# Kernel optimization log

Measured on AMD Instinct MI355X. Metric: run time of the kernel, lower is better.

## Reference

```python
import jax, jax.numpy as jnp
import numpy as np

DIM = 1024
NUM_HEADS = 16
HEAD_DIM = DIM // NUM_HEADS
SEQ = 2048
BATCH = 2


def setup_inputs() -> dict:
    key = jax.random.key(0)
    kx, kq, kk, kv, ko, kb = jax.random.split(key, 6)
    s = 0.02
    return {
        "x": jax.random.normal(kx, (BATCH, SEQ, DIM), dtype=jnp.float32),
        "W_q": jax.random.normal(kq, (DIM, DIM), dtype=jnp.float32) * s,
        "W_k": jax.random.normal(kk, (DIM, DIM), dtype=jnp.float32) * s,
        "W_v": jax.random.normal(kv, (DIM, DIM), dtype=jnp.float32) * s,
        "W_o": jax.random.normal(ko, (DIM, DIM), dtype=jnp.float32) * s,
        "b_o": jax.random.normal(kb, (DIM,), dtype=jnp.float32) * s,
    }


def reference(x, W_q, W_k, W_v, W_o, b_o):
    b, n, d = x.shape
    # Linear layers (torch Linear: y = x @ W.T); weights here stored as [out, in]
    q = jnp.einsum('bnd,ed->bne', x, W_q).reshape(b, n, NUM_HEADS, HEAD_DIM)
    k = jnp.einsum('bnd,ed->bne', x, W_k).reshape(b, n, NUM_HEADS, HEAD_DIM)
    v = jnp.einsum('bnd,ed->bne', x, W_v).reshape(b, n, NUM_HEADS, HEAD_DIM)
    # scores: [b, h, q, k]
    scores = jnp.einsum('bqhd,bkhd->bhqk', q, k)
    causal = jnp.tril(jnp.ones((n, n), dtype=bool))  # True = keep
    scores = jnp.where(causal, scores, -jnp.inf)
    weights = jax.nn.softmax(scores / jnp.sqrt(jnp.float32(HEAD_DIM)), axis=-1)
    ctx = jnp.einsum('bhqk,bkhd->bqhd', weights, v).reshape(b, n, d)
    return jnp.einsum('bnd,ed->bne', ctx, W_o) + b_o
```

## Files before the change

### kernel.cpp

```cpp
#include <hip/hip_runtime.h>
#include <hip/hip_bf16.h>

#define DIM 1024
#define NHEADS 16
#define HD 64
#define SEQ 2048
#define BATCH 2
#define MROWS (BATCH * SEQ)
#define MB (1024u * 1024u)
#define NT (SEQ / 64)

typedef __bf16 bf16x8 __attribute__((ext_vector_type(8)));
typedef float f32x4 __attribute__((ext_vector_type(4)));
typedef short short8 __attribute__((ext_vector_type(8)));

#define SCQ (0.125f * 1.44269504f)

__device__ __forceinline__ unsigned short f2bf(float f) {
    union { float f; unsigned u; } v; v.f = f;
    unsigned r = v.u + 0x7fffu + ((v.u >> 16) & 1u);
    return (unsigned short)(r >> 16);
}
__device__ __forceinline__ unsigned cvtpk(float lo, float hi) {
    unsigned r;
    asm("v_cvt_pk_bf16_f32 %0, %1, %2" : "=v"(r) : "v"(lo), "v"(hi));
    return r;
}

__device__ __forceinline__ void gld16(const unsigned short* g, unsigned short* l) {
    __builtin_amdgcn_global_load_lds(
        (const __attribute__((address_space(1))) void*)g,
        (__attribute__((address_space(3))) void*)l, 16, 0, 0);
}

#define VWAIT(n) asm volatile("s_waitcnt vmcnt(" #n ")" ::: "memory")
#define BARRIER  do { __builtin_amdgcn_s_barrier(); __builtin_amdgcn_sched_barrier(0); } while (0)

__global__ __launch_bounds__(256) void f2all_kernel(
    const float* __restrict__ x,
    const float* __restrict__ w0, const float* __restrict__ w1,
    const float* __restrict__ w2, const float* __restrict__ w3,
    unsigned short* __restrict__ xb,
    unsigned short* __restrict__ o0, unsigned short* __restrict__ o1,
    unsigned short* __restrict__ o2, unsigned short* __restrict__ o3)
{
    const float* in; unsigned short* out; int n4;
    switch (blockIdx.y) {
        case 0: in = x;  out = xb; n4 = (MROWS * DIM) / 4; break;
        case 1: in = w0; out = o0; n4 = (DIM * DIM) / 4;   break;
        case 2: in = w1; out = o1; n4 = (DIM * DIM) / 4;   break;
        case 3: in = w2; out = o2; n4 = (DIM * DIM) / 4;   break;
        default: in = w3; out = o3; n4 = (DIM * DIM) / 4;  break;
    }
    int i = blockIdx.x * 256 + threadIdx.x;
    if (i < n4) {
        float4 v = ((const float4*)in)[i];
        ushort4 o;
        o.x = f2bf(v.x); o.y = f2bf(v.y); o.z = f2bf(v.z); o.w = f2bf(v.w);
        ((ushort4*)out)[i] = o;
    }
}


#define GEMM_VARS(Aptr, Bptr)                                                  \
    __shared__ unsigned short As[3][128 * 32];                                 \
    __shared__ unsigned short Bs[3][128 * 32];                                 \
    const int tid  = threadIdx.x;                                              \
    const int lane = tid & 63;                                                 \
    const int wid  = tid >> 6;                                                 \
    const int wrow = wid >> 1, wcol = wid & 1;                                 \
    const int l15  = lane & 15;                                                \
    const int lhi  = lane >> 4;                                                \
    f32x4 acc[4][4] = {};                                                      \
    const int r0s = tid >> 2;                                                  \
    const int c0s = (tid & 3) ^ ((r0s >> 1) & 3);                              \
    const int r1s = (tid + 256) >> 2;                                          \
    const int c1s = (tid & 3) ^ ((r1s >> 1) & 3);                              \
    const unsigned short* gA0 = (Aptr) + (size_t)(row0 + r0s) * DIM + c0s * 8; \
    const unsigned short* gA1 = (Aptr) + (size_t)(row0 + r1s) * DIM + c1s * 8; \
    const unsigned short* gB0 = (Bptr) + (size_t)(col0 + r0s) * DIM + c0s * 8; \
    const unsigned short* gB1 = (Bptr) + (size_t)(col0 + r1s) * DIM + c1s * 8;

#define GEMM_STAGE(bi, kofs)                                                   \
    gld16(gA0 + (kofs), &As[bi][tid * 8]);                                     \
    gld16(gA1 + (kofs), &As[bi][(tid + 256) * 8]);                             \
    gld16(gB0 + (kofs), &Bs[bi][tid * 8]);                                     \
    gld16(gB1 + (kofs), &Bs[bi][(tid + 256) * 8]);

#define GEMM_COMPUTE(bi)                                                       \
    {   const unsigned short* Ac = &As[bi][0];                                 \
        const unsigned short* Bc = &Bs[bi][0];                                 \
        bf16x8 af[4], bfr[4];                                                  \
        _Pragma("unroll")                                                      \
        for (int m = 0; m < 4; m++) {                                          \
            int r = wrow * 64 + m * 16 + l15;                                  \
            int c = lhi ^ ((r >> 1) & 3);                                      \
            af[m] = *(const bf16x8*)&Ac[r * 32 + c * 8];                       \
        }                                                                      \
        _Pragma("unroll")                                                      \
        for (int n = 0; n < 4; n++) {                                          \
            int r = wcol * 64 + n * 16 + l15;                                  \
            int c = lhi ^ ((r >> 1) & 3);                                      \
            bfr[n] = *(const bf16x8*)&Bc[r * 32 + c * 8];                      \
        }                                                                      \
        __builtin_amdgcn_s_setprio(1);                                         \
        _Pragma("unroll")                                                      \
        for (int m = 0; m < 4; m++)                                            \
            _Pragma("unroll")                                                  \
            for (int n = 0; n < 4; n++)                                        \
                acc[m][n] = __builtin_amdgcn_mfma_f32_16x16x32_bf16(           \
                    af[m], bfr[n], acc[m][n], 0, 0, 0);                        \
        __builtin_amdgcn_s_setprio(0);                                         \
    }

#define GEMM_PIPELINE()                                                        \
    GEMM_STAGE(0, 0)                                                           \
    GEMM_STAGE(1, 32)                                                          \
    int bi = 0;                                                                \
    for (int k0 = 0; k0 + 96 <= DIM; k0 += 32) {                               \
        VWAIT(4);                                                              \
        BARRIER;                                                               \
        int b2 = bi + 2; if (b2 >= 3) b2 -= 3;                                 \
        GEMM_STAGE(b2, k0 + 64)                                                \
        GEMM_COMPUTE(bi)                                                       \
        bi = (bi + 1 == 3) ? 0 : bi + 1;                                       \
    }                                                                          \
    VWAIT(4);                                                                  \
    BARRIER;                                                                   \
    GEMM_COMPUTE(bi)                                                           \
    bi = (bi + 1 == 3) ? 0 : bi + 1;                                           \
    VWAIT(0);                                                                  \
    BARRIER;                                                                   \
    GEMM_COMPUTE(bi)

__global__ __launch_bounds__(256) void qkv_gemm(
    const unsigned short* __restrict__ A,
    const unsigned short* __restrict__ Wqb,
    const unsigned short* __restrict__ Wkb,
    const unsigned short* __restrict__ Wvb,
    unsigned short* __restrict__ Qb,
    unsigned short* __restrict__ Kbf,
    unsigned short* __restrict__ Vtb)
{
    const int lb  = ((int)blockIdx.x & 7) * 96 + ((int)blockIdx.x >> 3);
    const int xx  = lb % 24;
    const int yy  = lb / 24;
    const int sel = xx >> 3;
    const unsigned short* Bw = (sel == 0) ? Wqb : ((sel == 1) ? Wkb : Wvb);
    const int row0 = yy * 128;
    const int col0 = (xx & 7) * 128;

    GEMM_VARS(A, Bw)
    GEMM_PIPELINE()

    const int cr = lhi * 4;
    unsigned short* outRM = (sel == 0) ? Qb : Kbf;
    #pragma unroll
    for (int m = 0; m < 4; m++) {
        #pragma unroll
        for (int n = 0; n < 4; n++) {
            #pragma unroll
            for (int j = 0; j < 4; j++) {
                int gr = row0 + wrow * 64 + m * 16 + cr + j;
                int gc = col0 + wcol * 64 + n * 16 + l15;
                float v = acc[m][n][j];
                if (sel == 0) v *= SCQ;
                unsigned short hv = f2bf(v);
                if (sel < 2) {
                    outRM[(size_t)gr * DIM + gc] = hv;
                } else {
                    int bb = gr >> 11, s = gr & 2047;
                    int hh = gc >> 6,  d = gc & 63;
                    Vtb[(((size_t)bb * NHEADS + hh) * HD + d) * SEQ + s] = hv;
                }
            }
        }
    }
}

__global__ __launch_bounds__(256) void o_gemm(
    const unsigned short* __restrict__ A,
    const unsigned short* __restrict__ Bw,
    float* __restrict__ Cp,
    const float* __restrict__ bias)
{
    __shared__ unsigned short As[3][64 * 32];
    __shared__ unsigned short Bs[3][128 * 32];

    const int lb  = ((int)blockIdx.x & 7) * 64 + ((int)blockIdx.x >> 3);
    const int xx  = lb % 8;
    const int yy  = lb / 8;
    const int row0 = yy * 64;
    const int col0 = xx * 128;

    const int tid  = threadIdx.x;
    const int lane = tid & 63;
    const int wid  = tid >> 6;
    const int wrow = wid >> 1, wcol = wid & 1;
    const int l15  = lane & 15;
    const int lhi  = lane >> 4;
    f32x4 acc[2][4] = {};

    const int r0s = tid >> 2;
    const int c0s = (tid & 3) ^ ((r0s >> 1) & 3);
    const int r1s = (tid + 256) >> 2;
    const int c1s = (tid & 3) ^ ((r1s >> 1) & 3);
    const unsigned short* gA0 = A  + (size_t)(row0 + r0s) * DIM + c0s * 8;
    const unsigned short* gB0 = Bw + (size_t)(col0 + r0s) * DIM + c0s * 8;
    const unsigned short* gB1 = Bw + (size_t)(col0 + r1s) * DIM + c1s * 8;

#define OSTAGE(bi, kofs)                                     \
    gld16(gA0 + (kofs), &As[bi][tid * 8]);                   \
    gld16(gB0 + (kofs), &Bs[bi][tid * 8]);                   \
    gld16(gB1 + (kofs), &Bs[bi][(tid + 256) * 8]);

#define OCOMPUTE(bi)                                                           \
    {   const unsigned short* Ac = &As[bi][0];                                 \
        const unsigned short* Bc = &Bs[bi][0];                                 \
        bf16x8 af[2], bfr[4];                                                  \
        _Pragma("unroll")                                                      \
        for (int m = 0; m < 2; m++) {                                          \
            int r = wrow * 32 + m * 16 + l15;                                  \
            int c = lhi ^ ((r >> 1) & 3);                                      \
            af[m] = *(const bf16x8*)&Ac[r * 32 + c * 8];                       \
        }                                                                      \
        _Pragma("unroll")                                                      \
        for (int n = 0; n < 4; n++) {                                          \
            int r = wcol * 64 + n * 16 + l15;                                  \
            int c = lhi ^ ((r >> 1) & 3);                                      \
            bfr[n] = *(const bf16x8*)&Bc[r * 32 + c * 8];                      \
        }                                                                      \
        __builtin_amdgcn_s_setprio(1);                                         \
        _Pragma("unroll")                                                      \
        for (int m = 0; m < 2; m++)                                            \
            _Pragma("unroll")                                                  \
            for (int n = 0; n < 4; n++)                                        \
                acc[m][n] = __builtin_amdgcn_mfma_f32_16x16x32_bf16(           \
                    af[m], bfr[n], acc[m][n], 0, 0, 0);                        \
        __builtin_amdgcn_s_setprio(0);                                         \
    }

    OSTAGE(0, 0)
    OSTAGE(1, 32)
    int bi = 0;
    for (int k0 = 0; k0 + 96 <= DIM; k0 += 32) {
        VWAIT(3);
        BARRIER;
        int b2 = bi + 2; if (b2 >= 3) b2 -= 3;
        OSTAGE(b2, k0 + 64)
        OCOMPUTE(bi)
        bi = (bi + 1 == 3) ? 0 : bi + 1;
    }
    VWAIT(3);
    BARRIER;
    OCOMPUTE(bi)
    bi = (bi + 1 == 3) ? 0 : bi + 1;
    VWAIT(0);
    BARRIER;
    OCOMPUTE(bi)
#undef OSTAGE
#undef OCOMPUTE

    const int cr = lhi * 4;
    #pragma unroll
    for (int m = 0; m < 2; m++) {
        #pragma unroll
        for (int n = 0; n < 4; n++) {
            #pragma unroll
            for (int j = 0; j < 4; j++) {
                int gr = row0 + wrow * 32 + m * 16 + cr + j;
                int gc = col0 + wcol * 64 + n * 16 + l15;
                Cp[(size_t)gr * DIM + gc] = acc[m][n][j] + bias[gc];
            }
        }
    }
}

#define ATTN_COMPUTE(bi, t)                                                    \
    {   const unsigned short* Kc = &Ks[bi][0];                                 \
        const unsigned short* Vc = &Vs[bi][0];                                 \
        f32x4 sacc[4] = {};                                                    \
        __builtin_amdgcn_s_setprio(1);                                         \
        _Pragma("unroll")                                                      \
        for (int ks = 0; ks < 2; ++ks) {                                       \
            bf16x8 bq = ks ? aq1 : aq0;                                        \
            _Pragma("unroll")                                                  \
            for (int nt = 0; nt < 4; nt++) {                                   \
                int r = nt * 16 + l15;                                         \
                int c = (ks * 4 + lhi) ^ (r & 7);                              \
                bf16x8 ak = *(const bf16x8*)&Kc[r * 64 + c * 8];               \
                sacc[nt] = __builtin_amdgcn_mfma_f32_16x16x32_bf16(            \
                    ak, bq, sacc[nt], 0, 0, 0);                                \
            }                                                                  \
        }                                                                      \
        __builtin_amdgcn_s_setprio(0);                                         \
        const bool diag = ((t) == qblk);                                       \
        _Pragma("unroll")                                                      \
        for (int nt = 0; nt < 4; nt++) {                                       \
            float pv[4];                                                       \
            _Pragma("unroll")                                                  \
            for (int j = 0; j < 4; j++) {                                      \
                bool msk = diag && (nt * 16 + lhi * 4 + j > (w & 3) * 16 + l15); \
                pv[j] = msk ? 0.f : exp2f(sacc[nt][j]);                        \
            }                                                                  \
            *(uint2*)&Ps[w][l15][nt * 16 + lhi * 4] =                          \
                make_uint2(cvtpk(pv[0], pv[1]), cvtpk(pv[2], pv[3]));          \
        }                                                                      \
        __builtin_amdgcn_s_setprio(1);                                         \
        _Pragma("unroll")                                                      \
        for (int ks = 0; ks < 2; ++ks) {                                       \
            bf16x8 ap = *(const bf16x8*)&Ps[w][l15][ks * 32 + lhi * 8];        \
            _Pragma("unroll")                                                  \
            for (int dt = 0; dt < 4; dt++) {                                   \
                int r = dt * 16 + l15;                                         \
                int c = (ks * 4 + lhi) ^ (r & 7);                              \
                bf16x8 bv = *(const bf16x8*)&Vc[r * 64 + c * 8];               \
                octx[dt] = __builtin_amdgcn_mfma_f32_16x16x32_bf16(            \
                    ap, bv, octx[dt], 0, 0, 0);                                \
            }                                                                  \
            octxS = __builtin_amdgcn_mfma_f32_16x16x32_bf16(ap, vones, octxS, 0, 0, 0); \
        }                                                                      \
        __builtin_amdgcn_s_setprio(0);                                         \
    }

__global__ __launch_bounds__(512) void attn_kernel(
    const unsigned short* __restrict__ Q,
    const unsigned short* __restrict__ Kb,
    const unsigned short* __restrict__ Vt,
    unsigned short* __restrict__ Ctx)
{
    __shared__ unsigned short Ks[3][64 * 64];
    __shared__ unsigned short Vs[3][64 * 64];
    __shared__ unsigned short Ps[8][16][72];

    const int tid  = threadIdx.x;
    const int lane = tid & 63;
    const int w    = tid >> 6;
    const int bid  = (int)blockIdx.x;
    const int half = bid >> 8;
    const int idx  = bid & 255;
    const int h    = idx & 15;
    const int b    = (idx >> 4) & 1;
    const int slot = idx >> 5;
    const int p    = half ? slot : (15 - slot);
    const int l15  = lane & 15;
    const int lhi  = lane >> 4;

    const int qblk   = 2 * p + (w >> 2);
    const int qw     = qblk * 64 + (w & 3) * 16;
    const int ntiles = 2 * p + 2;

    const size_t qrow = ((size_t)b * SEQ + qw + l15) * DIM + h * HD;
    bf16x8 aq0 = *(const bf16x8*)(Q + qrow + lhi * 8);
    bf16x8 aq1 = *(const bf16x8*)(Q + qrow + 32 + lhi * 8);

    const int srow = tid >> 3;
    const int sc16 = (tid & 7) ^ (srow & 7);
    const unsigned short* gK = Kb + ((size_t)b * SEQ + srow) * DIM + h * HD + sc16 * 8;
    const unsigned short* gV = Vt + (((size_t)b * NHEADS + h) * HD + srow) * SEQ + sc16 * 8;

    bf16x8 vones;
    #pragma unroll
    for (int i = 0; i < 8; i++) vones[i] = (__bf16)1.0f;

    f32x4 octx[4] = {};
    f32x4 octxS = {};

    gld16(gK,                    &Ks[0][tid * 8]);
    gld16(gV,                    &Vs[0][tid * 8]);
    gld16(gK + (size_t)64 * DIM, &Ks[1][tid * 8]);
    gld16(gV + 64,               &Vs[1][tid * 8]);

    int bi = 0;
    for (int t = 0; t < ntiles; ++t) {
        if (t < ntiles - 1) { VWAIT(2); } else { VWAIT(0); }
        BARRIER;
        if (t + 2 < ntiles) {
            int b2 = bi + 2; if (b2 >= 3) b2 -= 3;
            gld16(gK + (size_t)(t + 2) * 64 * DIM, &Ks[b2][tid * 8]);
            gld16(gV + (size_t)(t + 2) * 64,       &Vs[b2][tid * 8]);
        }
        if (t <= qblk) ATTN_COMPUTE(bi, t);
        bi = (bi + 1 == 3) ? 0 : bi + 1;
    }

    #pragma unroll
    for (int j = 0; j < 4; j++) {
        float inv = 1.0f / octxS[j];
        #pragma unroll
        for (int dt = 0; dt < 4; dt++) {
            Ctx[((size_t)b * SEQ + qw + lhi * 4 + j) * DIM + h * HD + dt * 16 + l15] =
                f2bf(octx[dt][j] * inv);
        }
    }
}

extern "C" void kernel_launch(void* const* d_in, const int* in_sizes, int n_in,
                              void* d_out, int out_size, void* d_ws, size_t ws_size,
                              hipStream_t stream) {
    const float* x  = (const float*)d_in[0];
    const float* Wq = (const float*)d_in[1];
    const float* Wk = (const float*)d_in[2];
    const float* Wv = (const float*)d_in[3];
    const float* Wo = (const float*)d_in[4];
    const float* bo = (const float*)d_in[5];

    char* ws = (char*)d_ws;
    unsigned short* xb   = (unsigned short*)(ws + 0 * MB);
    unsigned short* Wqb  = (unsigned short*)(ws + 8 * MB);
    unsigned short* Wkb  = (unsigned short*)(ws + 10 * MB);
    unsigned short* Wvb  = (unsigned short*)(ws + 12 * MB);
    unsigned short* Wob  = (unsigned short*)(ws + 14 * MB);
    unsigned short* Qb   = (unsigned short*)(ws + 16 * MB);
    unsigned short* Kbf  = (unsigned short*)(ws + 24 * MB);
    unsigned short* Vtb  = (unsigned short*)(ws + 32 * MB);
    unsigned short* ctxb = (unsigned short*)(ws + 40 * MB);

    f2all_kernel<<<dim3(4096, 5), 256, 0, stream>>>(x, Wq, Wk, Wv, Wo,
                                                    xb, Wqb, Wkb, Wvb, Wob);

    qkv_gemm<<<768, 256, 0, stream>>>(xb, Wqb, Wkb, Wvb, Qb, Kbf, Vtb);

    attn_kernel<<<512, 512, 0, stream>>>(Qb, Kbf, Vtb, ctxb);

    o_gemm<<<512, 256, 0, stream>>>(ctxb, Wob, (float*)d_out, bo);
}
```

Measured before the change: 119.3 us.

## Software-pipeline attention loop: compute next tile's QK while doing current softmax and PV

New measurement: 119.6 us. Within noise of the previous version (+0.2%).

```diff
diff --git a/kernel.cpp b/kernel.cpp
--- a/kernel.cpp
+++ b/kernel.cpp
@@ -276,24 +276,24 @@
     }
 }
 
-#define ATTN_COMPUTE(bi, t)                                                    \
-    {   const unsigned short* Kc = &Ks[bi][0];                                 \
-        const unsigned short* Vc = &Vs[bi][0];                                 \
-        f32x4 sacc[4] = {};                                                    \
-        __builtin_amdgcn_s_setprio(1);                                         \
-        _Pragma("unroll")                                                      \
-        for (int ks = 0; ks < 2; ++ks) {                                       \
-            bf16x8 bq = ks ? aq1 : aq0;                                        \
-            _Pragma("unroll")                                                  \
-            for (int nt = 0; nt < 4; nt++) {                                   \
-                int r = nt * 16 + l15;                                         \
-                int c = (ks * 4 + lhi) ^ (r & 7);                              \
-                bf16x8 ak = *(const bf16x8*)&Kc[r * 64 + c * 8];               \
-                sacc[nt] = __builtin_amdgcn_mfma_f32_16x16x32_bf16(            \
-                    ak, bq, sacc[nt], 0, 0, 0);                                \
-            }                                                                  \
-        }                                                                      \
-        __builtin_amdgcn_s_setprio(0);                                         \
+
+#define ATTN_QK(SOUT, bK)                                                      \
+    {   const unsigned short* Kc = &Ks[bK][0];                                 \
+        _Pragma("unroll")                                                      \
+        for (int nt = 0; nt < 4; nt++) {                                       \
+            int r  = nt * 16 + l15;                                            \
+            int ca = lhi ^ (r & 7);                                            \
+            int cb = (4 + lhi) ^ (r & 7);                                      \
+            bf16x8 ak0 = *(const bf16x8*)&Kc[r * 64 + ca * 8];                 \
+            bf16x8 ak1 = *(const bf16x8*)&Kc[r * 64 + cb * 8];                 \
+            f32x4 zz = {0.f, 0.f, 0.f, 0.f};                                   \
+            SOUT[nt] = __builtin_amdgcn_mfma_f32_16x16x32_bf16(ak0, aq0, zz, 0, 0, 0); \
+            SOUT[nt] = __builtin_amdgcn_mfma_f32_16x16x32_bf16(ak1, aq1, SOUT[nt], 0, 0, 0); \
+        }                                                                      \
+    }
+
+#define ATTN_SMPV(SIN, bV, t)                                                  \
+    {   const unsigned short* Vc = &Vs[bV][0];                                 \
         const bool diag = ((t) == qblk);                                       \
         _Pragma("unroll")                                                      \
         for (int nt = 0; nt < 4; nt++) {                                       \
@@ -301,15 +301,15 @@
             _Pragma("unroll")                                                  \
             for (int j = 0; j < 4; j++) {                                      \
                 bool msk = diag && (nt * 16 + lhi * 4 + j > (w & 3) * 16 + l15); \
-                pv[j] = msk ? 0.f : exp2f(sacc[nt][j]);                        \
+                pv[j] = msk ? 0.f : exp2f(SIN[nt][j]);                         \
             }                                                                  \
             *(uint2*)&Ps[w][l15][nt * 16 + lhi * 4] =                          \
                 make_uint2(cvtpk(pv[0], pv[1]), cvtpk(pv[2], pv[3]));          \
         }                                                                      \
-        __builtin_amdgcn_s_setprio(1);                                         \
         _Pragma("unroll")                                                      \
         for (int ks = 0; ks < 2; ++ks) {                                       \
             bf16x8 ap = *(const bf16x8*)&Ps[w][l15][ks * 32 + lhi * 8];        \
+            __builtin_amdgcn_s_setprio(1);                                     \
             _Pragma("unroll")                                                  \
             for (int dt = 0; dt < 4; dt++) {                                   \
                 int r = dt * 16 + l15;                                         \
@@ -319,9 +319,22 @@
                     ap, bv, octx[dt], 0, 0, 0);                                \
             }                                                                  \
             octxS = __builtin_amdgcn_mfma_f32_16x16x32_bf16(ap, vones, octxS, 0, 0, 0); \
-        }                                                                      \
-        __builtin_amdgcn_s_setprio(0);                                         \
-    }
+            __builtin_amdgcn_s_setprio(0);                                     \
+        }                                                                      \
+    }
+
+#define ATTN_ITER(t, bcur, bnxt, bpre, SIN, SOUT)                              \
+    BARRIER;                                                                   \
+    if ((t) + 2 < ntiles) {                                                    \
+        gld16(gK + (size_t)((t) + 2) * 64 * DIM, &Ks[bpre][tid * 8]);          \
+        gld16(gV + (size_t)((t) + 2) * 64,       &Vs[bpre][tid * 8]);          \
+        VWAIT(2);                                                              \
+    } else {                                                                   \
+        VWAIT(0);                                                              \
+    }                                                                          \
+    BARRIER;                                                                   \
+    if ((t) + 1 <= qblk) ATTN_QK(SOUT, bnxt)                                   \
+    if ((t) <= qblk)     ATTN_SMPV(SIN, bcur, t)
 
 __global__ __launch_bounds__(512) void attn_kernel(
     const unsigned short* __restrict__ Q,
@@ -365,23 +378,23 @@
 
     f32x4 octx[4] = {};
     f32x4 octxS = {};
+    f32x4 sA[4], sB[4];
 
     gld16(gK,                    &Ks[0][tid * 8]);
     gld16(gV,                    &Vs[0][tid * 8]);
     gld16(gK + (size_t)64 * DIM, &Ks[1][tid * 8]);
     gld16(gV + 64,               &Vs[1][tid * 8]);
+    VWAIT(2);
+    BARRIER;
+    ATTN_QK(sA, 0)
 
     int bi = 0;
-    for (int t = 0; t < ntiles; ++t) {
-        if (t < ntiles - 1) { VWAIT(2); } else { VWAIT(0); }
-        BARRIER;
-        if (t + 2 < ntiles) {
-            int b2 = bi + 2; if (b2 >= 3) b2 -= 3;
-            gld16(gK + (size_t)(t + 2) * 64 * DIM, &Ks[b2][tid * 8]);
-            gld16(gV + (size_t)(t + 2) * 64,       &Vs[b2][tid * 8]);
-        }
-        if (t <= qblk) ATTN_COMPUTE(bi, t);
-        bi = (bi + 1 == 3) ? 0 : bi + 1;
+    for (int t = 0; t < ntiles; t += 2) {
+        int b1 = bi + 1; if (b1 >= 3) b1 -= 3;
+        int b2 = bi + 2; if (b2 >= 3) b2 -= 3;
+        ATTN_ITER(t,     bi, b1, b2, sA, sB)
+        ATTN_ITER(t + 1, b1, b2, bi, sB, sA)
+        bi = b2;
     }
 
     #pragma unroll
```

## Give each attention wave 32 query rows and halve block size with double buffering

Applied to the files above, without the earlier changes.

After: 128.1 us. +7.4%, slower.

```diff
diff --git a/kernel.cpp b/kernel.cpp
--- a/kernel.cpp
+++ b/kernel.cpp
@@ -276,62 +276,15 @@
     }
 }
 
-#define ATTN_COMPUTE(bi, t)                                                    \
-    {   const unsigned short* Kc = &Ks[bi][0];                                 \
-        const unsigned short* Vc = &Vs[bi][0];                                 \
-        f32x4 sacc[4] = {};                                                    \
-        __builtin_amdgcn_s_setprio(1);                                         \
-        _Pragma("unroll")                                                      \
-        for (int ks = 0; ks < 2; ++ks) {                                       \
-            bf16x8 bq = ks ? aq1 : aq0;                                        \
-            _Pragma("unroll")                                                  \
-            for (int nt = 0; nt < 4; nt++) {                                   \
-                int r = nt * 16 + l15;                                         \
-                int c = (ks * 4 + lhi) ^ (r & 7);                              \
-                bf16x8 ak = *(const bf16x8*)&Kc[r * 64 + c * 8];               \
-                sacc[nt] = __builtin_amdgcn_mfma_f32_16x16x32_bf16(            \
-                    ak, bq, sacc[nt], 0, 0, 0);                                \
-            }                                                                  \
-        }                                                                      \
-        __builtin_amdgcn_s_setprio(0);                                         \
-        const bool diag = ((t) == qblk);                                       \
-        _Pragma("unroll")                                                      \
-        for (int nt = 0; nt < 4; nt++) {                                       \
-            float pv[4];                                                       \
-            _Pragma("unroll")                                                  \
-            for (int j = 0; j < 4; j++) {                                      \
-                bool msk = diag && (nt * 16 + lhi * 4 + j > (w & 3) * 16 + l15); \
-                pv[j] = msk ? 0.f : exp2f(sacc[nt][j]);                        \
-            }                                                                  \
-            *(uint2*)&Ps[w][l15][nt * 16 + lhi * 4] =                          \
-                make_uint2(cvtpk(pv[0], pv[1]), cvtpk(pv[2], pv[3]));          \
-        }                                                                      \
-        __builtin_amdgcn_s_setprio(1);                                         \
-        _Pragma("unroll")                                                      \
-        for (int ks = 0; ks < 2; ++ks) {                                       \
-            bf16x8 ap = *(const bf16x8*)&Ps[w][l15][ks * 32 + lhi * 8];        \
-            _Pragma("unroll")                                                  \
-            for (int dt = 0; dt < 4; dt++) {                                   \
-                int r = dt * 16 + l15;                                         \
-                int c = (ks * 4 + lhi) ^ (r & 7);                              \
-                bf16x8 bv = *(const bf16x8*)&Vc[r * 64 + c * 8];               \
-                octx[dt] = __builtin_amdgcn_mfma_f32_16x16x32_bf16(            \
-                    ap, bv, octx[dt], 0, 0, 0);                                \
-            }                                                                  \
-            octxS = __builtin_amdgcn_mfma_f32_16x16x32_bf16(ap, vones, octxS, 0, 0, 0); \
-        }                                                                      \
-        __builtin_amdgcn_s_setprio(0);                                         \
-    }
-
-__global__ __launch_bounds__(512) void attn_kernel(
+__global__ __launch_bounds__(256) void attn_kernel(
     const unsigned short* __restrict__ Q,
     const unsigned short* __restrict__ Kb,
     const unsigned short* __restrict__ Vt,
     unsigned short* __restrict__ Ctx)
 {
-    __shared__ unsigned short Ks[3][64 * 64];
-    __shared__ unsigned short Vs[3][64 * 64];
-    __shared__ unsigned short Ps[8][16][72];
+    __shared__ unsigned short Ks[2][64 * 64];
+    __shared__ unsigned short Vs[2][64 * 64];
+    __shared__ unsigned short Ps[4][32][72];
 
     const int tid  = threadIdx.x;
     const int lane = tid & 63;
@@ -346,51 +299,117 @@
     const int l15  = lane & 15;
     const int lhi  = lane >> 4;
 
-    const int qblk   = 2 * p + (w >> 2);
-    const int qw     = qblk * 64 + (w & 3) * 16;
+    const int qbase  = 128 * p + 32 * w;
+    const int qblkw  = 2 * p + (w >> 1);
+    const int qrel0  = 32 * (w & 1);
     const int ntiles = 2 * p + 2;
 
-    const size_t qrow = ((size_t)b * SEQ + qw + l15) * DIM + h * HD;
-    bf16x8 aq0 = *(const bf16x8*)(Q + qrow + lhi * 8);
-    bf16x8 aq1 = *(const bf16x8*)(Q + qrow + 32 + lhi * 8);
-
-    const int srow = tid >> 3;
-    const int sc16 = (tid & 7) ^ (srow & 7);
-    const unsigned short* gK = Kb + ((size_t)b * SEQ + srow) * DIM + h * HD + sc16 * 8;
-    const unsigned short* gV = Vt + (((size_t)b * NHEADS + h) * HD + srow) * SEQ + sc16 * 8;
+    bf16x8 aq[2][2];
+    #pragma unroll
+    for (int g = 0; g < 2; g++) {
+        const size_t qrow = ((size_t)b * SEQ + qbase + 16 * g + l15) * DIM + h * HD;
+        aq[g][0] = *(const bf16x8*)(Q + qrow + lhi * 8);
+        aq[g][1] = *(const bf16x8*)(Q + qrow + 32 + lhi * 8);
+    }
+
+    const int r0  = tid >> 3;
+    const int sc  = (tid & 7) ^ (r0 & 7);
+    const unsigned short* gK0 = Kb + ((size_t)b * SEQ + r0)      * DIM + h * HD + sc * 8;
+    const unsigned short* gK1 = Kb + ((size_t)b * SEQ + r0 + 32) * DIM + h * HD + sc * 8;
+    const unsigned short* gV0 = Vt + (((size_t)b * NHEADS + h) * HD + r0)      * SEQ + sc * 8;
+    const unsigned short* gV1 = Vt + (((size_t)b * NHEADS + h) * HD + r0 + 32) * SEQ + sc * 8;
+
+#define ASTAGE(bi, t)                                                          \
+    gld16(gK0 + (size_t)(t) * 64 * DIM, &Ks[bi][tid * 8]);                     \
+    gld16(gK1 + (size_t)(t) * 64 * DIM, &Ks[bi][(tid + 256) * 8]);             \
+    gld16(gV0 + (size_t)(t) * 64,       &Vs[bi][tid * 8]);                     \
+    gld16(gV1 + (size_t)(t) * 64,       &Vs[bi][(tid + 256) * 8]);
 
     bf16x8 vones;
     #pragma unroll
     for (int i = 0; i < 8; i++) vones[i] = (__bf16)1.0f;
 
-    f32x4 octx[4] = {};
-    f32x4 octxS = {};
-
-    gld16(gK,                    &Ks[0][tid * 8]);
-    gld16(gV,                    &Vs[0][tid * 8]);
-    gld16(gK + (size_t)64 * DIM, &Ks[1][tid * 8]);
-    gld16(gV + 64,               &Vs[1][tid * 8]);
-
-    int bi = 0;
+    f32x4 octx[2][4] = {};
+    f32x4 octxS[2] = {};
+
+    ASTAGE(0, 0)
+    __syncthreads();
+
+    int cur = 0;
     for (int t = 0; t < ntiles; ++t) {
-        if (t < ntiles - 1) { VWAIT(2); } else { VWAIT(0); }
-        BARRIER;
-        if (t + 2 < ntiles) {
-            int b2 = bi + 2; if (b2 >= 3) b2 -= 3;
-            gld16(gK + (size_t)(t + 2) * 64 * DIM, &Ks[b2][tid * 8]);
-            gld16(gV + (size_t)(t + 2) * 64,       &Vs[b2][tid * 8]);
+        if (t + 1 < ntiles) ASTAGE(cur ^ 1, t + 1)
+        if (t <= qblkw) {
+            const unsigned short* Kc = &Ks[cur][0];
+            const unsigned short* Vc = &Vs[cur][0];
+
+            f32x4 sacc[2][4] = {};
+            __builtin_amdgcn_s_setprio(1);
+            #pragma unroll
+            for (int nt = 0; nt < 4; nt++) {
+                int r  = nt * 16 + l15;
+                bf16x8 ak0 = *(const bf16x8*)&Kc[r * 64 + (lhi ^ (r & 7)) * 8];
+                bf16x8 ak1 = *(const bf16x8*)&Kc[r * 64 + (((4 + lhi) ^ (r & 7))) * 8];
+                #pragma unroll
+                for (int g = 0; g < 2; g++) {
+                    sacc[g][nt] = __builtin_amdgcn_mfma_f32_16x16x32_bf16(ak0, aq[g][0], sacc[g][nt], 0, 0, 0);
+                    sacc[g][nt] = __builtin_amdgcn_mfma_f32_16x16x32_bf16(ak1, aq[g][1], sacc[g][nt], 0, 0, 0);
+                }
+            }
+            __builtin_amdgcn_s_setprio(0);
+
+            const bool diag = (t == qblkw);
+            #pragma unroll
+            for (int g = 0; g < 2; g++) {
+                const int qrel = qrel0 + 16 * g + l15;
+                #pragma unroll
+                for (int nt = 0; nt < 4; nt++) {
+                    float pv[4];
+                    #pragma unroll
+                    for (int j = 0; j < 4; j++) {
+                        bool msk = diag && (nt * 16 + lhi * 4 + j > qrel);
+                        pv[j] = msk ? 0.f : exp2f(sacc[g][nt][j]);
+                    }
+                    *(uint2*)&Ps[w][16 * g + l15][nt * 16 + lhi * 4] =
+                        make_uint2(cvtpk(pv[0], pv[1]), cvtpk(pv[2], pv[3]));
+                }
+            }
+
+            #pragma unroll
+            for (int ks = 0; ks < 2; ++ks) {
+                bf16x8 bv[4];
+                #pragma unroll
+                for (int dt = 0; dt < 4; dt++) {
+                    int r = dt * 16 + l15;
+                    bv[dt] = *(const bf16x8*)&Vc[r * 64 + (((ks * 4 + lhi) ^ (r & 7))) * 8];
+                }
+                __builtin_amdgcn_s_setprio(1);
+                #pragma unroll
+                for (int g = 0; g < 2; g++) {
+                    bf16x8 ap = *(const bf16x8*)&Ps[w][16 * g + l15][ks * 32 + lhi * 8];
+                    #pragma unroll
+                    for (int dt = 0; dt < 4; dt++)
+                        octx[g][dt] = __builtin_amdgcn_mfma_f32_16x16x32_bf16(ap, bv[dt], octx[g][dt], 0, 0, 0);
+                    octxS[g] = __builtin_amdgcn_mfma_f32_16x16x32_bf16(ap, vones, octxS[g], 0, 0, 0);
+                }
+                __builtin_amdgcn_s_setprio(0);
+            }
         }
-        if (t <= qblk) ATTN_COMPUTE(bi, t);
-        bi = (bi + 1 == 3) ? 0 : bi + 1;
-    }
+        __syncthreads();
+        cur ^= 1;
+    }
+#undef ASTAGE
 
     #pragma unroll
-    for (int j = 0; j < 4; j++) {
-        float inv = 1.0f / octxS[j];
+    for (int g = 0; g < 2; g++) {
         #pragma unroll
-        for (int dt = 0; dt < 4; dt++) {
-            Ctx[((size_t)b * SEQ + qw + lhi * 4 + j) * DIM + h * HD + dt * 16 + l15] =
-                f2bf(octx[dt][j] * inv);
+        for (int j = 0; j < 4; j++) {
+            float inv = 1.0f / octxS[g][j];
+            int q = qbase + 16 * g + lhi * 4 + j;
+            #pragma unroll
+            for (int dt = 0; dt < 4; dt++) {
+                Ctx[((size_t)b * SEQ + q) * DIM + h * HD + dt * 16 + l15] =
+                    f2bf(octx[g][dt][j] * inv);
+            }
         }
     }
 }
@@ -421,7 +440,7 @@
 
     qkv_gemm<<<768, 256, 0, stream>>>(xb, Wqb, Wkb, Wvb, Qb, Kbf, Vtb);
 
-    attn_kernel<<<512, 512, 0, stream>>>(Qb, Kbf, Vtb, ctxb);
+    attn_kernel<<<512, 256, 0, stream>>>(Qb, Kbf, Vtb, ctxb);
 
     o_gemm<<<512, 256, 0, stream>>>(ctxb, Wob, (float*)d_out, bo);
 }
```
